# Kernel optimization log

Measured on AMD Instinct MI355X. Metric: run time of the kernel, lower is better.

Reference implementation:

```python
import jax, jax.numpy as jnp
import numpy as np

N_NODES = 50000
N_EDGES = 1600000
HIDDEN = 128
HEADS = 8
HEAD_DIM = HIDDEN // HEADS


def setup_inputs() -> dict:
    key = jax.random.key(0)
    ks = jax.random.split(key, 6)
    s = 1.0 / np.sqrt(HIDDEN)
    return {
        "h":   jax.random.normal(ks[0], (N_NODES, HIDDEN), dtype=jnp.float32),
        "W_Q": jax.random.normal(ks[1], (HIDDEN, HIDDEN), dtype=jnp.float32) * s,
        "b_Q": jnp.zeros((HIDDEN,), jnp.float32),
        "W_K": jax.random.normal(ks[2], (HIDDEN, HIDDEN), dtype=jnp.float32) * s,
        "b_K": jnp.zeros((HIDDEN,), jnp.float32),
        "W_V": jax.random.normal(ks[3], (HIDDEN, HIDDEN), dtype=jnp.float32) * s,
        "b_V": jnp.zeros((HIDDEN,), jnp.float32),
        "src": jax.random.randint(ks[4], (N_EDGES,), 0, N_NODES, dtype=jnp.int32),
        "dst": jax.random.randint(ks[5], (N_EDGES,), 0, N_NODES, dtype=jnp.int32),
    }


def _gcn_conv(h, W, b, src, dst, norm_out, norm_in):
    # DGL GraphConv, norm='both', in_feats == out_feats -> aggregate then matmul
    feat = h * norm_out[:, None]                                   # [N, H]
    agg = jax.ops.segment_sum(feat[src], dst, num_segments=N_NODES)  # [N, H]
    agg = agg * norm_in[:, None]
    return agg @ W + b


def reference(h, W_Q, b_Q, W_K, b_K, W_V, b_V, src, dst):
    ones = jnp.ones((N_EDGES,), jnp.float32)
    deg_out = jnp.clip(jax.ops.segment_sum(ones, src, num_segments=N_NODES), 1.0)
    deg_in = jnp.clip(jax.ops.segment_sum(ones, dst, num_segments=N_NODES), 1.0)
    norm_out = jax.lax.rsqrt(deg_out)
    norm_in = jax.lax.rsqrt(deg_in)

    Q = jax.nn.relu(_gcn_conv(h, W_Q, b_Q, src, dst, norm_out, norm_in))
    K = jax.nn.relu(_gcn_conv(h, W_K, b_K, src, dst, norm_out, norm_in))
    V = jax.nn.relu(_gcn_conv(h, W_V, b_V, src, dst, norm_out, norm_in))

    Qh = Q.reshape(N_NODES, HEADS, HEAD_DIM)
    Kh = K.reshape(N_NODES, HEADS, HEAD_DIM)
    Vh = V.reshape(N_NODES, HEADS, HEAD_DIM)

    # per-edge attention: score_e = <K[src], Q[dst]> per head, exp-clamped
    scale = np.sqrt(HEAD_DIM).astype(np.float32)
    score = jnp.sum(Kh[src] * Qh[dst], axis=-1)                    # [E, heads]
    score = jnp.exp(jnp.clip(score / scale, -10.0, 10.0))

    wV = jax.ops.segment_sum(Vh[src] * score[:, :, None], dst, num_segments=N_NODES)  # [N, heads, d]
    z = jax.ops.segment_sum(score, dst, num_segments=N_NODES)     # [N, heads]
    return wV / (z[:, :, None] + 1e-6)
```

## Files before the change

kernel.cpp:

```cpp
#include <hip/hip_runtime.h>

#define N_NODES 50000
#define N_EDGES 1600000
#define CAP 64
#define OVF_CAP 8192

#define BIN_SHIFT 7
#define BIN_NODES 128
#define NBINS 391
#define BIN_CAP 5120
#define EPB 4096

#define O_CNTO   0
#define O_CNTI   50000
#define O_OVFN   100000
#define O_OVF    100002
#define O_BINC   116400
#define O_BUCKET 120000
#define O_HB     3320000
#define O_AGGB   6520000
#define O_WT     9720000
#define O_QB     9750000
#define O_KV     12950000
#define O_PAIRS  3320000

typedef unsigned int uint;
typedef __attribute__((ext_vector_type(8))) short short8;
typedef __attribute__((ext_vector_type(4))) float floatx4;

union U16 { uint4 u; short8 s; };

__device__ __forceinline__ uint f2bf2(float a, float b) {
    uint ua = __float_as_uint(a); ua = (ua + 0x7fffu + ((ua >> 16) & 1u)) >> 16;
    uint ub = __float_as_uint(b); ub = (ub + 0x7fffu + ((ub >> 16) & 1u)) >> 16;
    return ua | (ub << 16);
}
__device__ __forceinline__ float bflo(uint u) { return __uint_as_float(u << 16); }
__device__ __forceinline__ float bfhi(uint u) { return __uint_as_float(u & 0xffff0000u); }

template<int CTRL>
__device__ __forceinline__ float dpp_add8(float x) {
    int t = __builtin_amdgcn_update_dpp(0, __float_as_int(x), CTRL, 0xF, 0xF, true);
    return x + __int_as_float(t);
}
__device__ __forceinline__ float dpp_xor1(float x) {
    int t = __builtin_amdgcn_update_dpp(0, __float_as_int(x), 0xB1, 0xF, 0xF, true);
    return __int_as_float(t);
}

__global__ __launch_bounds__(256) void k_part(const int* __restrict__ src,
                                              const int* __restrict__ dst,
                                              int* cnt_out,
                                              int* bin_cnt,
                                              int2* __restrict__ pairs) {
    __shared__ int hist[NBINS];
    __shared__ int base[NBINS];
    const int t = threadIdx.x;
    const int e0 = blockIdx.x * EPB;

    for (int b = t; b < NBINS; b += 256) hist[b] = 0;
    __syncthreads();

    #pragma unroll
    for (int i = 0; i < EPB / 256; ++i) {
        int e = e0 + i * 256 + t;
        if (e < N_EDGES) {
            int d = dst[e];
            atomicAdd(&hist[d >> BIN_SHIFT], 1);
            atomicAdd(&cnt_out[src[e]], 1);
        }
    }
    __syncthreads();

    for (int b = t; b < NBINS; b += 256) {
        base[b] = atomicAdd(&bin_cnt[b], hist[b]);
        hist[b] = 0;
    }
    __syncthreads();

    #pragma unroll
    for (int i = 0; i < EPB / 256; ++i) {
        int e = e0 + i * 256 + t;
        if (e < N_EDGES) {
            int d = dst[e], s = src[e];
            int bin = d >> BIN_SHIFT;
            int idx = base[bin] + atomicAdd(&hist[bin], 1);
            if (idx < BIN_CAP)
                pairs[(size_t)bin * BIN_CAP + idx] = make_int2(d, s);
        }
    }
}

__global__ __launch_bounds__(256) void k_bins(const int* __restrict__ bin_cnt,
                                              const int2* __restrict__ pairs,
                                              int* __restrict__ cnt_in,
                                              int* __restrict__ bucket,
                                              int* ovf_n, int2* __restrict__ ovf) {
    __shared__ int lcnt[BIN_NODES];
    const int b = blockIdx.x;
    const int t = threadIdx.x;
    for (int i = t; i < BIN_NODES; i += 256) lcnt[i] = 0;
    __syncthreads();

    const int nb = min(bin_cnt[b], BIN_CAP);
    const int2* pp = pairs + (size_t)b * BIN_CAP;
    for (int i = t; i < nb; i += 256) {
        int2 p = pp[i];
        int pos = atomicAdd(&lcnt[p.x & (BIN_NODES - 1)], 1);
        if (pos < CAP) {
            bucket[((size_t)p.x << 6) + pos] = p.y;
        } else {
            int o = atomicAdd(ovf_n, 1);
            if (o < OVF_CAP) ovf[o] = p;
        }
    }
    __syncthreads();

    const int node0 = b << BIN_SHIFT;
    for (int i = t; i < BIN_NODES; i += 256) {
        int n = node0 + i;
        if (n < N_NODES) cnt_in[n] = lcnt[i];
    }
}

__global__ __launch_bounds__(256) void k_wt(const float* __restrict__ WQ,
                                            const float* __restrict__ WK,
                                            const float* __restrict__ WV,
                                            uint* __restrict__ wt) {
    int idx = blockIdx.x * 256 + threadIdx.x;
    if (idx < 3 * 8192) {
        int y = idx >> 13;
        int rem = idx & 8191;
        int k2 = rem >> 7;
        int n  = rem & 127;
        const float* W = (y == 0) ? WQ : (y == 1) ? WK : WV;
        float a = W[(2 * k2) * 128 + n];
        float b = W[(2 * k2 + 1) * 128 + n];
        wt[(y << 13) + (n << 6) + k2] = f2bf2(a, b);
    }
}

__global__ __launch_bounds__(256) void k_hb(const float* __restrict__ h,
                                            const int* __restrict__ cnt_out,
                                            uint* __restrict__ hb) {
    int idx = blockIdx.x * 256 + threadIdx.x;
    if (idx < N_NODES * 64) {
        int n = idx >> 6;
        float no = rsqrtf(fmaxf((float)cnt_out[n], 1.0f));
        float2 hv = *(const float2*)(h + ((size_t)idx << 1));
        hb[idx] = f2bf2(hv.x * no, hv.y * no);
    }
}

__global__ __launch_bounds__(256) void k_agg(
    const int* __restrict__ cnt_in, const int* __restrict__ bucket,
    const int* __restrict__ ovf_n, const int2* __restrict__ ovf,
    const uint* __restrict__ hb, uint* __restrict__ aggb)
{
    int n = blockIdx.x * 4 + (threadIdx.x >> 6);
    int lane = threadIdx.x & 63;
    int cnt = cnt_in[n];
    int m = min(cnt, CAP);
    const int* b = bucket + ((size_t)n << 6);
    int s_own = b[lane];
    float ax = 0.f, ay = 0.f;

    if (m > 0) {
        uint uA[16], uB[16];
        const int nb = (m + 15) >> 4;
        const int mm1 = m - 1;

#define AGLD(P, base) do { _Pragma("unroll")                                   \
        for (int j = 0; j < 16; ++j) {                                         \
            int sj = __builtin_amdgcn_readlane(s_own, min((base) + j, mm1));   \
            P[j] = hb[((uint)sj << 6) + (uint)lane];                           \
        } } while (0)
#define AGCMP(P, base) do { _Pragma("unroll")                                  \
        for (int j = 0; j < 16; ++j) {                                         \
            if ((base) + j < m) { ax += bflo(P[j]); ay += bfhi(P[j]); }        \
        } } while (0)

        AGLD(uA, 0);
        int t = 0;
        while (t + 1 < nb) {
            AGLD(uB, (t + 1) << 4);
            AGCMP(uA, t << 4);
            ++t;
            if (t + 1 < nb) {
                AGLD(uA, (t + 1) << 4);
                AGCMP(uB, t << 4);
                ++t;
            } else {
                AGCMP(uB, t << 4);
                ++t;
                break;
            }
        }
        if (t < nb) { AGCMP(uA, t << 4); }
#undef AGLD
#undef AGCMP
    }

    if (cnt > CAP) {
        int on = min(*ovf_n, OVF_CAP);
        for (int j = 0; j < on; ++j) {
            int2 p = ovf[j];
            if (p.x == n) {
                uint u = hb[((uint)p.y << 6) + (uint)lane];
                ax += bflo(u);
                ay += bfhi(u);
            }
        }
    }
    float ni = rsqrtf(fmaxf((float)cnt, 1.0f));
    aggb[((size_t)n << 6) + lane] = f2bf2(ax * ni, ay * ni);
}

__global__ __launch_bounds__(256) void k_qkv(
    const uint* __restrict__ aggb, const uint* __restrict__ wt,
    const float* __restrict__ bQ, const float* __restrict__ bK,
    const float* __restrict__ bV,
    uint* __restrict__ qb, uint* __restrict__ kv)
{
    const int y = blockIdx.y;
    const int row0 = blockIdx.x * 128;
    const float* bias = (y == 0) ? bQ : (y == 1) ? bK : bV;

    __shared__ uint sA[128 * 68];

    const int t = threadIdx.x;
    for (int idx = t; idx < 128 * 16; idx += 256) {
        int r = idx >> 4, c4 = (idx & 15) << 2;
        int row = row0 + r;
        uint4 v = make_uint4(0u, 0u, 0u, 0u);
        if (row < N_NODES) v = *(const uint4*)(aggb + ((size_t)row << 6) + c4);
        *(uint4*)(&sA[r * 68 + c4]) = v;
    }
    __syncthreads();

    const int wave = t >> 6;
    const int lane = t & 63;
    const int mrow = lane & 15;
    const int kq   = lane >> 4;
    const int mbase = wave * 32;
    const uint* wty = wt + (y << 13);

    floatx4 acc[2][8];
    for (int a = 0; a < 2; ++a)
        for (int b = 0; b < 8; ++b)
            acc[a][b] = (floatx4){0.f, 0.f, 0.f, 0.f};

    for (int kc = 0; kc < 128; kc += 32) {
        int koff = (kc >> 1) + (kq << 2);
        short8 afr[2], bfr[8];
        for (int mt = 0; mt < 2; ++mt) {
            U16 u; u.u = *(const uint4*)(&sA[(mbase + mt * 16 + mrow) * 68 + koff]);
            afr[mt] = u.s;
        }
        for (int nt = 0; nt < 8; ++nt) {
            U16 u; u.u = *(const uint4*)(wty + ((nt * 16 + mrow) << 6) + koff);
            bfr[nt] = u.s;
        }
        for (int mt = 0; mt < 2; ++mt)
            for (int nt = 0; nt < 8; ++nt)
                acc[mt][nt] = __builtin_amdgcn_mfma_f32_16x16x32_bf16(
                    afr[mt], bfr[nt], acc[mt][nt], 0, 0, 0);
    }

    if (y == 0) {
        for (int mt = 0; mt < 2; ++mt) {
            int rbase = row0 + mbase + mt * 16 + kq * 4;
            for (int nt = 0; nt < 8; ++nt) {
                int c = nt * 16 + mrow;
                float bv = bias[c];
                for (int r = 0; r < 4; ++r) {
                    float v = fmaxf(acc[mt][nt][r] + bv, 0.f);
                    float pv = dpp_xor1(v);
                    int row = rbase + r;
                    if (((lane & 1) == 0) && row < N_NODES)
                        qb[((size_t)row << 6) + (c >> 1)] = f2bf2(v, pv);
                }
            }
        }
    } else {
        const int vo = (y == 2) ? 1 : 0;
        for (int mt = 0; mt < 2; ++mt) {
            int rbase = row0 + mbase + mt * 16 + kq * 4;
            for (int nt = 0; nt < 8; ++nt) {
                int c = nt * 16 + mrow;
                float bv = bias[c];
                for (int r = 0; r < 4; ++r) {
                    float v = fmaxf(acc[mt][nt][r] + bv, 0.f);
                    float pv = dpp_xor1(v);
                    int row = rbase + r;
                    if (((lane & 1) == 0) && row < N_NODES)
                        kv[((size_t)row << 7) + c + vo] = f2bf2(v, pv);
                }
            }
        }
    }
}

#define SC_MUL 0.36067376022243085f
#define SC_CLP 14.426950408889634f

__device__ __forceinline__ void attn_step(uint2 kvp, float qx, float qy,
                                          float& ax, float& ay, float& zacc) {
    float p = bflo(kvp.x) * qx + bfhi(kvp.x) * qy;
    p = dpp_add8<0xB1>(p);
    p = dpp_add8<0x4E>(p);
    p = dpp_add8<0x141>(p);
    float tt = fminf(fmaxf(p * SC_MUL, -SC_CLP), SC_CLP);
    float sc;
    asm("v_exp_f32 %0, %1" : "=v"(sc) : "v"(tt));
    ax += bflo(kvp.y) * sc;
    ay += bfhi(kvp.y) * sc;
    zacc += sc;
}

__global__ __launch_bounds__(256) void k_attn(
    const int* __restrict__ cnt_in, const int* __restrict__ bucket,
    const int* __restrict__ ovf_n, const int2* __restrict__ ovf,
    const uint* __restrict__ qb, const uint* __restrict__ kv,
    float* __restrict__ out)
{
    int n = blockIdx.x * 4 + (threadIdx.x >> 6);
    int lane = threadIdx.x & 63;
    int cnt = cnt_in[n];
    int m = min(cnt, CAP);
    const int* b = bucket + ((size_t)n << 6);
    int s_own = b[lane];

    uint qu = qb[((size_t)n << 6) + lane];
    float qx = bflo(qu), qy = bfhi(qu);
    float ax = 0.f, ay = 0.f, zacc = 0.f;
    const uint loff = (uint)(lane << 1);

    if (m > 0) {
        uint2 pA[8], pB[8];
        const int nb = (m + 7) >> 3;
        const int mm1 = m - 1;

#define KVLD(P, base) do { _Pragma("unroll")                                   \
        for (int j = 0; j < 8; ++j) {                                          \
            int sj = __builtin_amdgcn_readlane(s_own, min((base) + j, mm1));   \
            P[j] = *(const uint2*)(kv + (((uint)sj << 7) + loff));             \
        } } while (0)
#define KVCMP(P, base) do { _Pragma("unroll")                                  \
        for (int j = 0; j < 8; ++j) {                                          \
            if ((base) + j < m) attn_step(P[j], qx, qy, ax, ay, zacc);         \
        } } while (0)

        KVLD(pA, 0);
        int t = 0;
        while (t + 1 < nb) {
            KVLD(pB, (t + 1) << 3);
            KVCMP(pA, t << 3);
            ++t;
            if (t + 1 < nb) {
                KVLD(pA, (t + 1) << 3);
                KVCMP(pB, t << 3);
                ++t;
            } else {
                KVCMP(pB, t << 3);
                ++t;
                break;
            }
        }
        if (t < nb) { KVCMP(pA, t << 3); }
#undef KVLD
#undef KVCMP
    }

    if (cnt > CAP) {
        int on = min(*ovf_n, OVF_CAP);
        for (int j = 0; j < on; ++j) {
            int2 pr = ovf[j];
            if (pr.x == n) {
                uint2 p = *(const uint2*)(kv + (((uint)pr.y << 7) + loff));
                attn_step(p, qx, qy, ax, ay, zacc);
            }
        }
    }

    float inv = 1.0f / (zacc + 1e-6f);
    float2 o; o.x = ax * inv; o.y = ay * inv;
    *(float2*)(out + ((size_t)n << 7) + (lane << 1)) = o;
}

extern "C" void kernel_launch(void* const* d_in, const int* in_sizes, int n_in,
                              void* d_out, int out_size, void* d_ws, size_t ws_size,
                              hipStream_t stream) {
    const float* h   = (const float*)d_in[0];
    const float* WQ  = (const float*)d_in[1];
    const float* bQ  = (const float*)d_in[2];
    const float* WK  = (const float*)d_in[3];
    const float* bK  = (const float*)d_in[4];
    const float* WV  = (const float*)d_in[5];
    const float* bV  = (const float*)d_in[6];
    const int*   src = (const int*)d_in[7];
    const int*   dst = (const int*)d_in[8];
    float* out = (float*)d_out;
    float* ws  = (float*)d_ws;
    int*   wsi = (int*)d_ws;

    int*   cnt_out = wsi + O_CNTO;
    int*   cnt_in  = wsi + O_CNTI;
    int*   ovf_n   = wsi + O_OVFN;
    int2*  ovf     = (int2*)(wsi + O_OVF);
    int*   bin_cnt = wsi + O_BINC;
    int*   bucket  = wsi + O_BUCKET;
    int2*  pairs   = (int2*)(wsi + O_PAIRS);
    uint*  hb      = (uint*)(ws + O_HB);
    uint*  aggb    = (uint*)(ws + O_AGGB);
    uint*  wt      = (uint*)(ws + O_WT);
    uint*  qb      = (uint*)(ws + O_QB);
    uint*  kv      = (uint*)(ws + O_KV);

    hipMemsetAsync(wsi, 0, (O_BINC + NBINS) * sizeof(int), stream);

    k_wt<<<(3 * 8192 + 255) / 256, 256, 0, stream>>>(WQ, WK, WV, wt);

    k_part<<<(N_EDGES + EPB - 1) / EPB, 256, 0, stream>>>(src, dst, cnt_out,
                                                          bin_cnt, pairs);
    k_bins<<<NBINS, 256, 0, stream>>>(bin_cnt, pairs, cnt_in, bucket, ovf_n, ovf);

    k_hb<<<(N_NODES * 64 + 255) / 256, 256, 0, stream>>>(h, cnt_out, hb);

    k_agg<<<N_NODES / 4, 256, 0, stream>>>(cnt_in, bucket, ovf_n, ovf, hb, aggb);

    dim3 g_qkv((N_NODES + 127) / 128, 3);
    k_qkv<<<g_qkv, 256, 0, stream>>>(aggb, wt, bQ, bK, bV, qb, kv);

    k_attn<<<N_NODES / 4, 256, 0, stream>>>(cnt_in, bucket, ovf_n, ovf,
                                            qb, kv, out);
}
```

Measured before the change: 402.4 us.

## Restructure attention into persistent phased kernel that tiles source nodes for cache reuse

Replaces the one-wave-per-node attention kernel with a persistent kernel of 768 blocks. Each wave handles 17 destination nodes, and the kernel walks source-node ranges in 8 phases with a software grid barrier between them. All CUs then gather K/V rows from the same slice of source nodes at the same time, so the working set can stay in L2/MALL instead of being fetched at random. In exchange it adds barrier spin overhead and register pressure from 17 accumulator sets, loses the batched 8-deep prefetch, and relies on every block being co-resident (the spin has a timeout budget).

New measurement: 827.5 us. 2.06x slower.

```diff
diff --git a/kernel.cpp b/kernel.cpp
--- a/kernel.cpp
+++ b/kernel.cpp
@@ -11,11 +11,18 @@
 #define BIN_CAP 5120
 #define EPB 4096
 
+#define NBLK_C 768
+#define NWAVES_C 3072
+#define NSLOT 17
+#define NPH 8
+#define TILE_N 6250
+
 #define O_CNTO   0
 #define O_CNTI   50000
 #define O_OVFN   100000
 #define O_OVF    100002
 #define O_BINC   116400
+#define O_PHC    116800
 #define O_BUCKET 120000
 #define O_HB     3320000
 #define O_AGGB   6520000
@@ -25,6 +32,7 @@
 #define O_PAIRS  3320000
 
 typedef unsigned int uint;
+typedef unsigned long long ulong64;
 typedef __attribute__((ext_vector_type(8))) short short8;
 typedef __attribute__((ext_vector_type(4))) float floatx4;
 
@@ -318,74 +326,95 @@
     zacc += sc;
 }
 
-__global__ __launch_bounds__(256) void k_attn(
+
+#define SETUP(k)                                                               \
+    const int n##k = wg + (k) * NWAVES_C;                                      \
+    int s##k = 0;                                                              \
+    float qx##k = 0.f, qy##k = 0.f, ax##k = 0.f, ay##k = 0.f, z##k = 0.f;      \
+    ulong64 vm##k = 0ull;                                                      \
+    if (n##k < N_NODES) {                                                      \
+        int cnt_ = cnt_in[n##k];                                               \
+        int mm_ = min(cnt_, CAP);                                              \
+        s##k = bucket[((size_t)n##k << 6) + lane];                             \
+        uint qu_ = qb[((size_t)n##k << 6) + lane];                             \
+        qx##k = bflo(qu_); qy##k = bfhi(qu_);                                  \
+        vm##k = __ballot(lane < mm_);                                          \
+    }
+
+#define SLOT_PHASE(k)                                                          \
+    {                                                                          \
+        ulong64 msk = __ballot((uint)(s##k - lo) < (uint)TILE_N) & vm##k;      \
+        if (msk) {                                                             \
+            int j0 = __builtin_ctzll(msk); msk &= msk - 1;                     \
+            int sj0 = __builtin_amdgcn_readlane(s##k, j0);                     \
+            uint2 p0 = *(const uint2*)(kv + (((uint)sj0 << 7) + loff));        \
+            while (msk) {                                                      \
+                int j1 = __builtin_ctzll(msk); msk &= msk - 1;                 \
+                int sj1 = __builtin_amdgcn_readlane(s##k, j1);                 \
+                uint2 p1 = *(const uint2*)(kv + (((uint)sj1 << 7) + loff));    \
+                attn_step(p0, qx##k, qy##k, ax##k, ay##k, z##k);               \
+                p0 = p1;                                                       \
+            }                                                                  \
+            attn_step(p0, qx##k, qy##k, ax##k, ay##k, z##k);                   \
+        }                                                                      \
+    }
+
+#define FINISH(k)                                                              \
+    if (n##k < N_NODES) {                                                      \
+        int cnt_ = cnt_in[n##k];                                               \
+        if (cnt_ > CAP) {                             \
+            int on_ = min(*ovf_n, OVF_CAP);                                    \
+            for (int j2 = 0; j2 < on_; ++j2) {                                 \
+                int2 pr_ = ovf[j2];                                            \
+                if (pr_.x == n##k) {                                           \
+                    uint2 p_ = *(const uint2*)(kv + (((uint)pr_.y << 7) + loff)); \
+                    attn_step(p_, qx##k, qy##k, ax##k, ay##k, z##k);           \
+                }                                                              \
+            }                                                                  \
+        }                                                                      \
+        float inv_ = 1.0f / (z##k + 1e-6f);                                    \
+        float2 o_; o_.x = ax##k * inv_; o_.y = ay##k * inv_;                   \
+        *(float2*)(out + ((size_t)n##k << 7) + (lane << 1)) = o_;              \
+    }
+
+__global__ __launch_bounds__(256, 3) void k_attn_coop(
     const int* __restrict__ cnt_in, const int* __restrict__ bucket,
     const int* __restrict__ ovf_n, const int2* __restrict__ ovf,
     const uint* __restrict__ qb, const uint* __restrict__ kv,
-    float* __restrict__ out)
+    int* phc, float* __restrict__ out)
 {
-    int n = blockIdx.x * 4 + (threadIdx.x >> 6);
-    int lane = threadIdx.x & 63;
-    int cnt = cnt_in[n];
-    int m = min(cnt, CAP);
-    const int* b = bucket + ((size_t)n << 6);
-    int s_own = b[lane];
-
-    uint qu = qb[((size_t)n << 6) + lane];
-    float qx = bflo(qu), qy = bfhi(qu);
-    float ax = 0.f, ay = 0.f, zacc = 0.f;
+    const int lane = threadIdx.x & 63;
+    const int wg = blockIdx.x * 4 + (threadIdx.x >> 6);
     const uint loff = (uint)(lane << 1);
 
-    if (m > 0) {
-        uint2 pA[8], pB[8];
-        const int nb = (m + 7) >> 3;
-        const int mm1 = m - 1;
-
-#define KVLD(P, base) do { _Pragma("unroll")                                   \
-        for (int j = 0; j < 8; ++j) {                                          \
-            int sj = __builtin_amdgcn_readlane(s_own, min((base) + j, mm1));   \
-            P[j] = *(const uint2*)(kv + (((uint)sj << 7) + loff));             \
-        } } while (0)
-#define KVCMP(P, base) do { _Pragma("unroll")                                  \
-        for (int j = 0; j < 8; ++j) {                                          \
-            if ((base) + j < m) attn_step(P[j], qx, qy, ax, ay, zacc);         \
-        } } while (0)
-
-        KVLD(pA, 0);
-        int t = 0;
-        while (t + 1 < nb) {
-            KVLD(pB, (t + 1) << 3);
-            KVCMP(pA, t << 3);
-            ++t;
-            if (t + 1 < nb) {
-                KVLD(pA, (t + 1) << 3);
-                KVCMP(pB, t << 3);
-                ++t;
-            } else {
-                KVCMP(pB, t << 3);
-                ++t;
-                break;
+    SETUP(0)  SETUP(1)  SETUP(2)  SETUP(3)  SETUP(4)  SETUP(5)
+    SETUP(6)  SETUP(7)  SETUP(8)  SETUP(9)  SETUP(10) SETUP(11)
+    SETUP(12) SETUP(13) SETUP(14) SETUP(15) SETUP(16)
+
+    for (int ph = 0; ph < NPH; ++ph) {
+        const int lo = ph * TILE_N;
+        SLOT_PHASE(0)  SLOT_PHASE(1)  SLOT_PHASE(2)  SLOT_PHASE(3)
+        SLOT_PHASE(4)  SLOT_PHASE(5)  SLOT_PHASE(6)  SLOT_PHASE(7)
+        SLOT_PHASE(8)  SLOT_PHASE(9)  SLOT_PHASE(10) SLOT_PHASE(11)
+        SLOT_PHASE(12) SLOT_PHASE(13) SLOT_PHASE(14) SLOT_PHASE(15)
+        SLOT_PHASE(16)
+
+        if (ph + 1 < NPH) {
+            __syncthreads();
+            if (threadIdx.x == 0) {
+                atomicAdd(&phc[ph], 1);
+                int budget = 1 << 16;
+                while (__hip_atomic_load(&phc[ph], __ATOMIC_RELAXED,
+                                         __HIP_MEMORY_SCOPE_AGENT) < NBLK_C
+                       && --budget) { }
             }
-        }
-        if (t < nb) { KVCMP(pA, t << 3); }
-#undef KVLD
-#undef KVCMP
-    }
-
-    if (cnt > CAP) {
-        int on = min(*ovf_n, OVF_CAP);
-        for (int j = 0; j < on; ++j) {
-            int2 pr = ovf[j];
-            if (pr.x == n) {
-                uint2 p = *(const uint2*)(kv + (((uint)pr.y << 7) + loff));
-                attn_step(p, qx, qy, ax, ay, zacc);
-            }
-        }
-    }
-
-    float inv = 1.0f / (zacc + 1e-6f);
-    float2 o; o.x = ax * inv; o.y = ay * inv;
-    *(float2*)(out + ((size_t)n << 7) + (lane << 1)) = o;
+            __syncthreads();
+        }
+    }
+
+    FINISH(0)  FINISH(1)  FINISH(2)  FINISH(3)  FINISH(4)  FINISH(5)
+    FINISH(6)  FINISH(7)  FINISH(8)  FINISH(9)  FINISH(10) FINISH(11)
+    FINISH(12) FINISH(13) FINISH(14) FINISH(15) FINISH(16)
 }
 
 extern "C" void kernel_launch(void* const* d_in, const int* in_sizes, int n_in,
@@ -409,6 +438,7 @@
     int*   ovf_n   = wsi + O_OVFN;
     int2*  ovf     = (int2*)(wsi + O_OVF);
     int*   bin_cnt = wsi + O_BINC;
+    int*   phc     = wsi + O_PHC;
     int*   bucket  = wsi + O_BUCKET;
     int2*  pairs   = (int2*)(wsi + O_PAIRS);
     uint*  hb      = (uint*)(ws + O_HB);
@@ -417,7 +447,7 @@
     uint*  qb      = (uint*)(ws + O_QB);
     uint*  kv      = (uint*)(ws + O_KV);
 
-    hipMemsetAsync(wsi, 0, (O_BINC + NBINS) * sizeof(int), stream);
+    hipMemsetAsync(wsi, 0, (O_PHC + NPH) * sizeof(int), stream);
 
     k_wt<<<(3 * 8192 + 255) / 256, 256, 0, stream>>>(WQ, WK, WV, wt);
 
@@ -432,6 +462,6 @@
     dim3 g_qkv((N_NODES + 127) / 128, 3);
     k_qkv<<<g_qkv, 256, 0, stream>>>(aggb, wt, bQ, bK, bV, qb, kv);
 
-    k_attn<<<N_NODES / 4, 256, 0, stream>>>(cnt_in, bucket, ovf_n, ovf,
-                                            qb, kv, out);
-}
+    k_attn_coop<<<NBLK_C, 256, 0, stream>>>(cnt_in, bucket, ovf_n, ovf,
+                                            qb, kv, phc, out);
+}
```

## Split interleaved K/V buffer and compute attention in two gather passes

Applied to the files above, without the earlier changes.

Stores K and V in separate bf16 arrays instead of one interleaved row, and splits the attention kernel into a K pass that computes exp-scores into LDS and a V pass that reads them back and accumulates. The aim is to cut per-iteration register use for prefetch buffers and simplify loads. In exchange each neighbor row is gathered with two separate narrower loads across two serialized passes, adding load instructions and LDS traffic.

New measurement: 427.9 us. 1.06x slower.

```diff
diff --git a/kernel.cpp b/kernel.cpp
--- a/kernel.cpp
+++ b/kernel.cpp
@@ -21,10 +21,12 @@
 #define O_AGGB   6520000
 #define O_WT     9720000
 #define O_QB     9750000
-#define O_KV     12950000
+#define O_KB     12950000
+#define O_VB     16150000
 #define O_PAIRS  3320000
 
 typedef unsigned int uint;
+typedef unsigned long long ulong64;
 typedef __attribute__((ext_vector_type(8))) short short8;
 typedef __attribute__((ext_vector_type(4))) float floatx4;
 
@@ -220,11 +222,12 @@
     const uint* __restrict__ aggb, const uint* __restrict__ wt,
     const float* __restrict__ bQ, const float* __restrict__ bK,
     const float* __restrict__ bV,
-    uint* __restrict__ qb, uint* __restrict__ kv)
+    uint* __restrict__ qb, uint* __restrict__ kb, uint* __restrict__ vb)
 {
     const int y = blockIdx.y;
     const int row0 = blockIdx.x * 128;
     const float* bias = (y == 0) ? bQ : (y == 1) ? bK : bV;
+    uint* ob = (y == 0) ? qb : (y == 1) ? kb : vb;
 
     __shared__ uint sA[128 * 68];
 
@@ -267,35 +270,17 @@
                     afr[mt], bfr[nt], acc[mt][nt], 0, 0, 0);
     }
 
-    if (y == 0) {
-        for (int mt = 0; mt < 2; ++mt) {
-            int rbase = row0 + mbase + mt * 16 + kq * 4;
-            for (int nt = 0; nt < 8; ++nt) {
-                int c = nt * 16 + mrow;
-                float bv = bias[c];
-                for (int r = 0; r < 4; ++r) {
-                    float v = fmaxf(acc[mt][nt][r] + bv, 0.f);
-                    float pv = dpp_xor1(v);
-                    int row = rbase + r;
-                    if (((lane & 1) == 0) && row < N_NODES)
-                        qb[((size_t)row << 6) + (c >> 1)] = f2bf2(v, pv);
-                }
-            }
-        }
-    } else {
-        const int vo = (y == 2) ? 1 : 0;
-        for (int mt = 0; mt < 2; ++mt) {
-            int rbase = row0 + mbase + mt * 16 + kq * 4;
-            for (int nt = 0; nt < 8; ++nt) {
-                int c = nt * 16 + mrow;
-                float bv = bias[c];
-                for (int r = 0; r < 4; ++r) {
-                    float v = fmaxf(acc[mt][nt][r] + bv, 0.f);
-                    float pv = dpp_xor1(v);
-                    int row = rbase + r;
-                    if (((lane & 1) == 0) && row < N_NODES)
-                        kv[((size_t)row << 7) + c + vo] = f2bf2(v, pv);
-                }
+    for (int mt = 0; mt < 2; ++mt) {
+        int rbase = row0 + mbase + mt * 16 + kq * 4;
+        for (int nt = 0; nt < 8; ++nt) {
+            int c = nt * 16 + mrow;
+            float bv = bias[c];
+            for (int r = 0; r < 4; ++r) {
+                float v = fmaxf(acc[mt][nt][r] + bv, 0.f);
+                float pv = dpp_xor1(v);
+                int row = rbase + r;
+                if (((lane & 1) == 0) && row < N_NODES)
+                    ob[((size_t)row << 6) + (c >> 1)] = f2bf2(v, pv);
             }
         }
     }
@@ -303,29 +288,18 @@
 
 #define SC_MUL 0.36067376022243085f
 #define SC_CLP 14.426950408889634f
-
-__device__ __forceinline__ void attn_step(uint2 kvp, float qx, float qy,
-                                          float& ax, float& ay, float& zacc) {
-    float p = bflo(kvp.x) * qx + bfhi(kvp.x) * qy;
-    p = dpp_add8<0xB1>(p);
-    p = dpp_add8<0x4E>(p);
-    p = dpp_add8<0x141>(p);
-    float tt = fminf(fmaxf(p * SC_MUL, -SC_CLP), SC_CLP);
-    float sc;
-    asm("v_exp_f32 %0, %1" : "=v"(sc) : "v"(tt));
-    ax += bflo(kvp.y) * sc;
-    ay += bfhi(kvp.y) * sc;
-    zacc += sc;
-}
 
 __global__ __launch_bounds__(256) void k_attn(
     const int* __restrict__ cnt_in, const int* __restrict__ bucket,
     const int* __restrict__ ovf_n, const int2* __restrict__ ovf,
-    const uint* __restrict__ qb, const uint* __restrict__ kv,
-    float* __restrict__ out)
+    const uint* __restrict__ qb, const uint* __restrict__ kb,
+    const uint* __restrict__ vb, float* __restrict__ out)
 {
-    int n = blockIdx.x * 4 + (threadIdx.x >> 6);
-    int lane = threadIdx.x & 63;
+    __shared__ float sc_lds[4][CAP][8];
+
+    const int wv = threadIdx.x >> 6;
+    const int n = blockIdx.x * 4 + wv;
+    const int lane = threadIdx.x & 63;
     int cnt = cnt_in[n];
     int m = min(cnt, CAP);
     const int* b = bucket + ((size_t)n << 6);
@@ -334,42 +308,87 @@
     uint qu = qb[((size_t)n << 6) + lane];
     float qx = bflo(qu), qy = bfhi(qu);
     float ax = 0.f, ay = 0.f, zacc = 0.f;
-    const uint loff = (uint)(lane << 1);
+    const int head = lane >> 3;
 
     if (m > 0) {
-        uint2 pA[8], pB[8];
         const int nb = (m + 7) >> 3;
         const int mm1 = m - 1;
-
-#define KVLD(P, base) do { _Pragma("unroll")                                   \
+        uint pA[8], pB[8];
+
+#define KLD(P, base) do { _Pragma("unroll")                                    \
         for (int j = 0; j < 8; ++j) {                                          \
             int sj = __builtin_amdgcn_readlane(s_own, min((base) + j, mm1));   \
-            P[j] = *(const uint2*)(kv + (((uint)sj << 7) + loff));             \
-        } } while (0)
-#define KVCMP(P, base) do { _Pragma("unroll")                                  \
+            P[j] = kb[((uint)sj << 6) + (uint)lane];                           \
+        } } while (0)
+#define KCMP(P, base) do { _Pragma("unroll")                                   \
         for (int j = 0; j < 8; ++j) {                                          \
-            if ((base) + j < m) attn_step(P[j], qx, qy, ax, ay, zacc);         \
-        } } while (0)
-
-        KVLD(pA, 0);
+            if ((base) + j < m) {                                              \
+                float p_ = bflo(P[j]) * qx + bfhi(P[j]) * qy;                  \
+                p_ = dpp_add8<0xB1>(p_);                                       \
+                p_ = dpp_add8<0x4E>(p_);                                       \
+                p_ = dpp_add8<0x141>(p_);                                      \
+                float tt_ = fminf(fmaxf(p_ * SC_MUL, -SC_CLP), SC_CLP);        \
+                float sc_;                                                     \
+                asm("v_exp_f32 %0, %1" : "=v"(sc_) : "v"(tt_));                \
+                zacc += sc_;                                                   \
+                if ((lane & 7) == 0) sc_lds[wv][(base) + j][head] = sc_;       \
+            }                                                                  \
+        } } while (0)
+
+        KLD(pA, 0);
         int t = 0;
         while (t + 1 < nb) {
-            KVLD(pB, (t + 1) << 3);
-            KVCMP(pA, t << 3);
+            KLD(pB, (t + 1) << 3);
+            KCMP(pA, t << 3);
             ++t;
             if (t + 1 < nb) {
-                KVLD(pA, (t + 1) << 3);
-                KVCMP(pB, t << 3);
+                KLD(pA, (t + 1) << 3);
+                KCMP(pB, t << 3);
                 ++t;
             } else {
-                KVCMP(pB, t << 3);
+                KCMP(pB, t << 3);
                 ++t;
                 break;
             }
         }
-        if (t < nb) { KVCMP(pA, t << 3); }
-#undef KVLD
-#undef KVCMP
+        if (t < nb) { KCMP(pA, t << 3); }
+#undef KLD
+#undef KCMP
+
+
+#define VLD(P, base) do { _Pragma("unroll")                                    \
+        for (int j = 0; j < 8; ++j) {                                          \
+            int sj = __builtin_amdgcn_readlane(s_own, min((base) + j, mm1));   \
+            P[j] = vb[((uint)sj << 6) + (uint)lane];                           \
+        } } while (0)
+#define VCMP(P, base) do { _Pragma("unroll")                                   \
+        for (int j = 0; j < 8; ++j) {                                          \
+            if ((base) + j < m) {                                              \
+                float sc_ = sc_lds[wv][(base) + j][head];                      \
+                ax += bflo(P[j]) * sc_;                                        \
+                ay += bfhi(P[j]) * sc_;                                        \
+            }                                                                  \
+        } } while (0)
+
+        VLD(pA, 0);
+        t = 0;
+        while (t + 1 < nb) {
+            VLD(pB, (t + 1) << 3);
+            VCMP(pA, t << 3);
+            ++t;
+            if (t + 1 < nb) {
+                VLD(pA, (t + 1) << 3);
+                VCMP(pB, t << 3);
+                ++t;
+            } else {
+                VCMP(pB, t << 3);
+                ++t;
+                break;
+            }
+        }
+        if (t < nb) { VCMP(pA, t << 3); }
+#undef VLD
+#undef VCMP
     }
 
     if (cnt > CAP) {
@@ -377,8 +396,18 @@
         for (int j = 0; j < on; ++j) {
             int2 pr = ovf[j];
             if (pr.x == n) {
-                uint2 p = *(const uint2*)(kv + (((uint)pr.y << 7) + loff));
-                attn_step(p, qx, qy, ax, ay, zacc);
+                uint kk = kb[((uint)pr.y << 6) + (uint)lane];
+                uint vvv = vb[((uint)pr.y << 6) + (uint)lane];
+                float p = bflo(kk) * qx + bfhi(kk) * qy;
+                p = dpp_add8<0xB1>(p);
+                p = dpp_add8<0x4E>(p);
+                p = dpp_add8<0x141>(p);
+                float tt = fminf(fmaxf(p * SC_MUL, -SC_CLP), SC_CLP);
+                float sc;
+                asm("v_exp_f32 %0, %1" : "=v"(sc) : "v"(tt));
+                zacc += sc;
+                ax += bflo(vvv) * sc;
+                ay += bfhi(vvv) * sc;
             }
         }
     }
@@ -415,7 +444,8 @@
     uint*  aggb    = (uint*)(ws + O_AGGB);
     uint*  wt      = (uint*)(ws + O_WT);
     uint*  qb      = (uint*)(ws + O_QB);
-    uint*  kv      = (uint*)(ws + O_KV);
+    uint*  kb      = (uint*)(ws + O_KB);
+    uint*  vb      = (uint*)(ws + O_VB);
 
     hipMemsetAsync(wsi, 0, (O_BINC + NBINS) * sizeof(int), stream);
 
@@ -430,8 +460,8 @@
     k_agg<<<N_NODES / 4, 256, 0, stream>>>(cnt_in, bucket, ovf_n, ovf, hb, aggb);
 
     dim3 g_qkv((N_NODES + 127) / 128, 3);
-    k_qkv<<<g_qkv, 256, 0, stream>>>(aggb, wt, bQ, bK, bV, qb, kv);
+    k_qkv<<<g_qkv, 256, 0, stream>>>(aggb, wt, bQ, bK, bV, qb, kb, vb);
 
     k_attn<<<N_NODES / 4, 256, 0, stream>>>(cnt_in, bucket, ovf_n, ovf,
-                                            qb, kv, out);
-}
+                                            qb, kb, vb, out);
+}
```
